# Kernel tuning notes

Hardware: AMD Instinct MI355X
Metric: run time of the kernel (lower is better)

The kernel has to match this reference:

```python
import jax, jax.numpy as jnp
import numpy as np

VOCAB = 50257
D_MODEL = 1024
PAD_IDX = 0
B, L = 4, 4096


def setup_inputs() -> dict:
    key = jax.random.key(0)
    k1, k2, k3, k4, k5 = jax.random.split(key, 5)
    input_ids = jax.random.randint(k1, (B, L), 0, VOCAB, dtype=jnp.int64 if jax.config.jax_enable_x64 else jnp.int32)
    role_mask = jax.random.randint(k2, (B, L), 0, 2, dtype=input_ids.dtype)
    emb = jax.random.normal(k3, (VOCAB, D_MODEL), dtype=jnp.float32)
    emb = emb.at[PAD_IDX].set(0.0)  # padding_idx row is zero in nn.Embedding
    # nn.Linear weight has shape (out, in); y = x @ W.T
    scale = 1.0 / np.sqrt(D_MODEL)
    W0 = jax.random.uniform(k4, (D_MODEL, D_MODEL), dtype=jnp.float32, minval=-scale, maxval=scale)
    W1 = jax.random.uniform(k5, (D_MODEL, D_MODEL), dtype=jnp.float32, minval=-scale, maxval=scale)
    return {"input_ids": input_ids, "role_mask": role_mask, "emb": emb, "W0": W0, "W1": W1}


def reference(input_ids, role_mask, emb, W0, W1):
    # Embedding lookup: (B, L, D)
    x = emb[input_ids]
    # Per-role linear transform (2-expert routing); compute both, select by mask.
    y0 = jnp.einsum('bld,ed->ble', x, W0)
    y1 = jnp.einsum('bld,ed->ble', x, W1)
    out = jnp.where((role_mask == 1)[..., None], y1, y0)
    return out
```

## Files before the change

### kernel.cpp

```cpp
#include <hip/hip_runtime.h>
#include <hip/hip_bf16.h>


#define M_TOK   16384
#define DIM     1024
#define MT      128
#define NTIL    130
#define XROWS   (NTIL * MT)
#define BK      64
#define PBLK    64
#define WBLKS   2048

typedef __attribute__((ext_vector_type(8))) short short8;
typedef __attribute__((ext_vector_type(4))) float f32x4;
typedef __attribute__((ext_vector_type(4))) unsigned int uint32x4;

#define OFF_TOK  256
#define OFF_PERM 66816
#define OFF_WB   133376

static __device__ __forceinline__ unsigned short f2bf(float f) {
    unsigned int u = __float_as_uint(f);
    u += 0x7fffu + ((u >> 16) & 1u);
    return (unsigned short)(u >> 16);
}

static __device__ __forceinline__ unsigned int pk2(float a, float b) {
    __hip_bfloat162 h = __float22bfloat162_rn(make_float2(a, b));
    union { __hip_bfloat162 h; unsigned int u; } c;
    c.h = h;
    return c.u;
}

__global__ void k_pre(const int* __restrict__ role, const int* __restrict__ ids,
                      int* perm, int* tokid, int* cnt,
                      const float* __restrict__ W0, const float* __restrict__ W1,
                      unsigned short* __restrict__ Wb) {
    int b = blockIdx.x;
    if (b < PBLK) {
        int t = b * 256 + threadIdx.x;
        int row;
        if (role[t] == 1) { int s = atomicAdd(&cnt[1], 1); row = XROWS - 1 - s; }
        else              { int s = atomicAdd(&cnt[0], 1); row = s; }
        perm[row]  = t;
        tokid[row] = ids[t];
    } else {
        int idx = ((b - PBLK) * 256 + threadIdx.x) * 4;
        const float* src = (idx < 1048576) ? (W0 + idx) : (W1 + (idx - 1048576));
        float4 f = *(const float4*)src;
        *(ushort4*)(Wb + idx) = make_ushort4(f2bf(f.x), f2bf(f.y), f2bf(f.z), f2bf(f.w));
    }
}

__global__ __launch_bounds__(256, 3)
void k_gemm(const float* __restrict__ emb, const unsigned short* __restrict__ Wbu,
            const int* __restrict__ perm, const int* __restrict__ tokid,
            const int* __restrict__ cnt, float* __restrict__ out) {
    __shared__ float As[MT * BK];
    __shared__ short Bs[MT * BK];

    int f  = blockIdx.x;
    int mt = ((f >> 6) << 3) | (f & 7);
    int nt = (f >> 3) & 7;
    if (mt >= NTIL) return;

    int n0 = cnt[0], n1 = cnt[1];
    int T0 = (n0 + 127) >> 7, T1 = (n1 + 127) >> 7;
    int e, lo, hi;
    if (mt < T0)              { e = 0; lo = 0;            hi = n0;    }
    else if (mt >= NTIL - T1) { e = 1; lo = XROWS - n1;   hi = XROWS; }
    else return;

    const short* Bg = (const short*)Wbu + (size_t)e * DIM * DIM + (size_t)nt * MT * DIM;

    int tid  = threadIdx.x;
    int lane = tid & 63;
    int w    = tid >> 6;
    int wm   = w & 1, wn = w >> 1;
    int quad = lane >> 4, lq = lane & 15;

    unsigned int aoff[8];
#pragma unroll
    for (int q = 0; q < 8; ++q) {
        int row = 16 * q + 4 * w + quad;
        int kf  = (((lq >> 1) ^ (row & 7)) << 3) | ((lq & 1) << 2);
        aoff[q] = (unsigned int)tokid[mt * MT + row] * (DIM * 4) + kf * 4;
    }
    unsigned int boff[4];
#pragma unroll
    for (int q = 0; q < 4; ++q) {
        int s   = (q * 4 + w) * 64 + lane;
        int row = s >> 3;
        int kc  = (s & 7) ^ (row & 7);
        boff[q] = (unsigned int)(row * DIM + kc * 8) * 2;
    }

    f32x4 acc[4][4] = {};

    for (int k0 = 0; k0 < DIM; k0 += BK) {
#pragma unroll
        for (int q = 0; q < 8; ++q) {
            int s = (q * 4 + w) * 64 + lane;
            __builtin_amdgcn_global_load_lds(
                (const __attribute__((address_space(1))) unsigned int*)((const char*)emb + aoff[q] + k0 * 4),
                (__attribute__((address_space(3))) unsigned int*)(&As[s * 4]),
                16, 0, 0);
        }
#pragma unroll
        for (int q = 0; q < 4; ++q) {
            int s = (q * 4 + w) * 64 + lane;
            __builtin_amdgcn_global_load_lds(
                (const __attribute__((address_space(1))) unsigned int*)((const char*)Bg + boff[q] + k0 * 2),
                (__attribute__((address_space(3))) unsigned int*)(&Bs[s * 8]),
                16, 0, 0);
        }
        __syncthreads();

#pragma unroll
        for (int s = 0; s < 2; ++s) {
            int s4q = s * 4 + quad;
            short8 bv[4];
#pragma unroll
            for (int j = 0; j < 4; ++j) {
                int rb = wn * 64 + j * 16 + lq;
                bv[j] = *(const short8*)&Bs[(rb * 8 + (s4q ^ (rb & 7))) * 8];
            }
#pragma unroll
            for (int i = 0; i < 4; ++i) {
                int ra = wm * 64 + i * 16 + lq;
                int p  = s4q ^ (ra & 7);
                const f32x4* ap = (const f32x4*)&As[ra * BK + p * 8];
                f32x4 fl = ap[0], fh = ap[1];
                union { uint32x4 u; short8 v; } av;
                av.u[0] = pk2(fl[0], fl[1]);
                av.u[1] = pk2(fl[2], fl[3]);
                av.u[2] = pk2(fh[0], fh[1]);
                av.u[3] = pk2(fh[2], fh[3]);
#pragma unroll
                for (int j = 0; j < 4; ++j)
                    acc[i][j] = __builtin_amdgcn_mfma_f32_16x16x32_bf16(
                        av.v, bv[j], acc[i][j], 0, 0, 0);
            }
        }
        __syncthreads();
    }

    int colbase = nt * 128 + wn * 64 + lq;
#pragma unroll
    for (int i = 0; i < 4; ++i) {
#pragma unroll
        for (int r = 0; r < 4; ++r) {
            int mrow = mt * MT + wm * 64 + i * 16 + quad * 4 + r;
            if (mrow < lo || mrow >= hi) continue;
            int token = perm[mrow];
            float* o = out + (size_t)token * DIM + colbase;
#pragma unroll
            for (int j = 0; j < 4; ++j)
                o[j * 16] = acc[i][j][r];
        }
    }
}

extern "C" void kernel_launch(void* const* d_in, const int* in_sizes, int n_in,
                              void* d_out, int out_size, void* d_ws, size_t ws_size,
                              hipStream_t stream) {
    const int*   ids  = (const int*)d_in[0];
    const int*   role = (const int*)d_in[1];
    const float* emb  = (const float*)d_in[2];
    const float* W0   = (const float*)d_in[3];
    const float* W1   = (const float*)d_in[4];
    float*       out  = (float*)d_out;

    char* ws = (char*)d_ws;
    int* cnt   = (int*)ws;
    int* tokid = (int*)(ws + OFF_TOK);
    int* perm  = (int*)(ws + OFF_PERM);
    unsigned short* Wb = (unsigned short*)(ws + OFF_WB);

    hipMemsetAsync(ws, 0x00, OFF_PERM, stream);
    k_pre <<<PBLK + WBLKS, 256, 0, stream>>>(role, ids, perm, tokid, cnt, W0, W1, Wb);
    k_gemm<<<1088,         256, 0, stream>>>(emb, Wb, perm, tokid, cnt, out);
}
```

Measured before the change: 345.6 us.

## Convert A tile to bf16 in registers before staging into LDS

Embedding rows are now loaded into registers, converted to bf16 once, and written into a bf16 LDS tile, instead of being copied to LDS as fp32 via direct global-to-LDS loads and converted inside the MFMA loop. This halves LDS footprint and read traffic for A and removes the redundant per-wave conversions, since each A fragment was converted by both N-warps. The cost is that the A loads now pass through VGPRs, lose async direct-to-LDS behaviour, and add register pressure under the 3-blocks-per-SIMD bound.

```diff
diff --git a/kernel.cpp b/kernel.cpp
--- a/kernel.cpp
+++ b/kernel.cpp
@@ -13,7 +13,6 @@
 
 typedef __attribute__((ext_vector_type(8))) short short8;
 typedef __attribute__((ext_vector_type(4))) float f32x4;
-typedef __attribute__((ext_vector_type(4))) unsigned int uint32x4;
 
 #define OFF_TOK  256
 #define OFF_PERM 66816
@@ -56,7 +55,7 @@
 void k_gemm(const float* __restrict__ emb, const unsigned short* __restrict__ Wbu,
             const int* __restrict__ perm, const int* __restrict__ tokid,
             const int* __restrict__ cnt, float* __restrict__ out) {
-    __shared__ float As[MT * BK];
+    __shared__ short As[MT * BK];
     __shared__ short Bs[MT * BK];
 
     int f  = blockIdx.x;
@@ -72,6 +71,7 @@
     else return;
 
     const short* Bg = (const short*)Wbu + (size_t)e * DIM * DIM + (size_t)nt * MT * DIM;
+    const char*  embB = (const char*)emb;
 
     int tid  = threadIdx.x;
     int lane = tid & 63;
@@ -79,68 +79,64 @@
     int wm   = w & 1, wn = w >> 1;
     int quad = lane >> 4, lq = lane & 15;
 
-    unsigned int aoff[8];
+    unsigned int aoff[4];
+    unsigned int boff[4];
+    int sA[4];
 #pragma unroll
-    for (int q = 0; q < 8; ++q) {
-        int row = 16 * q + 4 * w + quad;
-        int kf  = (((lq >> 1) ^ (row & 7)) << 3) | ((lq & 1) << 2);
-        aoff[q] = (unsigned int)tokid[mt * MT + row] * (DIM * 4) + kf * 4;
-    }
-    unsigned int boff[4];
-#pragma unroll
-    for (int q = 0; q < 4; ++q) {
-        int s   = (q * 4 + w) * 64 + lane;
+    for (int i = 0; i < 4; ++i) {
+        int s   = (w * 4 + i) * 64 + lane;
         int row = s >> 3;
         int kc  = (s & 7) ^ (row & 7);
-        boff[q] = (unsigned int)(row * DIM + kc * 8) * 2;
+        sA[i]   = s;
+        aoff[i] = (unsigned int)tokid[mt * MT + row] * (DIM * 4) + (unsigned int)kc * 32;
+        boff[i] = (unsigned int)(row * DIM + kc * 8) * 2;
     }
 
     f32x4 acc[4][4] = {};
 
     for (int k0 = 0; k0 < DIM; k0 += BK) {
+        float4 fa[4][2];
 #pragma unroll
-        for (int q = 0; q < 8; ++q) {
-            int s = (q * 4 + w) * 64 + lane;
+        for (int i = 0; i < 4; ++i) {
+            const char* p = embB + aoff[i] + (unsigned int)k0 * 4;
+            fa[i][0] = *(const float4*)(p);
+            fa[i][1] = *(const float4*)(p + 16);
+        }
+#pragma unroll
+        for (int i = 0; i < 4; ++i) {
             __builtin_amdgcn_global_load_lds(
-                (const __attribute__((address_space(1))) unsigned int*)((const char*)emb + aoff[q] + k0 * 4),
-                (__attribute__((address_space(3))) unsigned int*)(&As[s * 4]),
+                (const __attribute__((address_space(1))) unsigned int*)((const char*)Bg + boff[i] + (unsigned int)k0 * 2),
+                (__attribute__((address_space(3))) unsigned int*)(&Bs[sA[i] * 8]),
                 16, 0, 0);
         }
 #pragma unroll
-        for (int q = 0; q < 4; ++q) {
-            int s = (q * 4 + w) * 64 + lane;
-            __builtin_amdgcn_global_load_lds(
-                (const __attribute__((address_space(1))) unsigned int*)((const char*)Bg + boff[q] + k0 * 2),
-                (__attribute__((address_space(3))) unsigned int*)(&Bs[s * 8]),
-                16, 0, 0);
+        for (int i = 0; i < 4; ++i) {
+            union { unsigned int u[4]; short8 v; } cv;
+            cv.u[0] = pk2(fa[i][0].x, fa[i][0].y);
+            cv.u[1] = pk2(fa[i][0].z, fa[i][0].w);
+            cv.u[2] = pk2(fa[i][1].x, fa[i][1].y);
+            cv.u[3] = pk2(fa[i][1].z, fa[i][1].w);
+            *(short8*)&As[sA[i] * 8] = cv.v;
         }
         __syncthreads();
 
 #pragma unroll
         for (int s = 0; s < 2; ++s) {
+            short8 av[4], bv[4];
             int s4q = s * 4 + quad;
-            short8 bv[4];
-#pragma unroll
-            for (int j = 0; j < 4; ++j) {
-                int rb = wn * 64 + j * 16 + lq;
-                bv[j] = *(const short8*)&Bs[(rb * 8 + (s4q ^ (rb & 7))) * 8];
-            }
 #pragma unroll
             for (int i = 0; i < 4; ++i) {
                 int ra = wm * 64 + i * 16 + lq;
-                int p  = s4q ^ (ra & 7);
-                const f32x4* ap = (const f32x4*)&As[ra * BK + p * 8];
-                f32x4 fl = ap[0], fh = ap[1];
-                union { uint32x4 u; short8 v; } av;
-                av.u[0] = pk2(fl[0], fl[1]);
-                av.u[1] = pk2(fl[2], fl[3]);
-                av.u[2] = pk2(fh[0], fh[1]);
-                av.u[3] = pk2(fh[2], fh[3]);
+                av[i] = *(const short8*)&As[(ra * 8 + (s4q ^ (ra & 7))) * 8];
+                int rb = wn * 64 + i * 16 + lq;
+                bv[i] = *(const short8*)&Bs[(rb * 8 + (s4q ^ (rb & 7))) * 8];
+            }
+#pragma unroll
+            for (int i = 0; i < 4; ++i)
 #pragma unroll
                 for (int j = 0; j < 4; ++j)
                     acc[i][j] = __builtin_amdgcn_mfma_f32_16x16x32_bf16(
-                        av.v, bv[j], acc[i][j], 0, 0, 0);
-            }
+                        av[i], bv[j], acc[i][j], 0, 0, 0);
         }
         __syncthreads();
     }
```

Measured after the change: 344.7 us. No clear change (-0.3%).
